# Optimization experiments

Measured on AMD Instinct MI355X. Metric: run time of the kernel, lower is better.

## Reference

```python
import jax, jax.numpy as jnp
import numpy as np

N_POI = 50000
D = 128
E = 400000
GCN_NUM = 3
HEADS = 8
B = 64
L = 100
LEAKY_SLOPE = 0.01
NORM_EPS = 1e-12


def setup_inputs() -> dict:
    key = jax.random.key(0)
    ks = jax.random.split(key, 11)
    return {
        "embeds": jax.random.normal(ks[0], (N_POI, D), jnp.float32) * 0.1,
        "gcn_W": jax.random.normal(ks[1], (GCN_NUM, D, D), jnp.float32) * (1.0 / np.sqrt(D)),
        "gcn_b": jnp.zeros((GCN_NUM, D), jnp.float32),
        "in_proj_w": jax.random.normal(ks[2], (3 * D, D), jnp.float32) * (1.0 / np.sqrt(D)),
        "in_proj_b": jnp.zeros((3 * D,), jnp.float32),
        "out_proj_w": jax.random.normal(ks[3], (D, D), jnp.float32) * (1.0 / np.sqrt(D)),
        "out_proj_b": jnp.zeros((D,), jnp.float32),
        "dist_vec": jax.random.uniform(ks[4], (E,), jnp.float32),
        "dist_edges": jax.random.randint(ks[5], (2, E), 0, N_POI),
        "x_idx": jax.random.randint(ks[6], (B * L,), 0, N_POI),
        "poi_idx": jax.random.randint(ks[7], (B,), 0, N_POI),
    }


def _self_attn(x, in_w, in_b, out_w, out_b):
    # x: [B, L, D]; standard nn.MultiheadAttention with Q=K=V=x, batch_first
    b, l, d = x.shape
    hd = d // HEADS
    qkv = x @ in_w.T + in_b                      # [B, L, 3D]
    q, k, v = jnp.split(qkv, 3, axis=-1)
    def heads(t):
        return t.reshape(b, l, HEADS, hd).transpose(0, 2, 1, 3)  # [B, H, L, hd]
    q, k, v = heads(q), heads(k), heads(v)
    scores = jnp.einsum('bhqd,bhkd->bhqk', q, k) / jnp.sqrt(jnp.asarray(hd, x.dtype))
    attn = jax.nn.softmax(scores, axis=-1)
    o = jnp.einsum('bhqk,bhkd->bhqd', attn, v).transpose(0, 2, 1, 3).reshape(b, l, d)
    return o @ out_w.T + out_b


def reference(embeds, gcn_W, gcn_b, in_proj_w, in_proj_b, out_proj_w, out_proj_b,
              dist_vec, dist_edges, x_idx, poi_idx):
    n_poi = embeds.shape[0]
    loop = jnp.arange(n_poi)
    # symmetrize edges + add self-loops (done in GeoGraph.__init__)
    rows = jnp.concatenate([dist_edges[0], dist_edges[1], loop])
    cols = jnp.concatenate([dist_edges[1], dist_edges[0], loop])
    dv = jnp.concatenate([dist_vec, dist_vec, jnp.zeros((n_poi,), dist_vec.dtype)])
    # symmetric degree normalization over destination (col) index
    deg = jax.ops.segment_sum(jnp.ones_like(dv), cols, num_segments=n_poi)
    dis = jnp.where(deg > 0, jax.lax.rsqrt(jnp.maximum(deg, 1e-12)), 0.0)
    w = jnp.exp(-dv ** 2) * dis[rows] * dis[cols]   # [E_full]

    enc = embeds
    for i in range(GCN_NUM):
        # sparse.mm: out[row] += w * enc[col]
        agg = jax.ops.segment_sum(w[:, None] * enc[cols], rows, num_segments=n_poi)
        enc = agg @ gcn_W[i].T + gcn_b[i]
        enc = jax.nn.leaky_relu(enc, LEAKY_SLOPE)
        enc = enc / jnp.maximum(jnp.linalg.norm(enc, axis=-1, keepdims=True), NORM_EPS)

    tar_embed = enc[poi_idx]                         # [B, D]
    geo_feat = enc[x_idx].reshape(B, L, D)           # equal-length sessions -> pad is a reshape
    attn_out = _self_attn(geo_feat, in_proj_w, in_proj_b, out_proj_w, out_proj_b)
    aggr_feat = attn_out.mean(axis=1)                # [B, D]
    return aggr_feat, tar_embed
```

## Files before the change

kernel.cpp:

```cpp
#include <hip/hip_runtime.h>
#include <math.h>

#define D 128
#define GCN_NUM 3
#define HEADS 8
#define HD 16
#define L_SEQ 100
#define LEAKY 0.01f
#define SC_BUCKETS 8

typedef __attribute__((ext_vector_type(8))) short short8v;
typedef __attribute__((ext_vector_type(4))) float f32x4;

__device__ __forceinline__ unsigned f2bf(float x) {
  unsigned u = __float_as_uint(x);
  return (u + 0x7FFFu + ((u >> 16) & 1u)) >> 16;
}
__device__ __forceinline__ float bflo2f(unsigned u) { return __uint_as_float(u << 16); }
__device__ __forceinline__ float bfhi2f(unsigned u) { return __uint_as_float(u & 0xFFFF0000u); }


__global__ void prep(const float* __restrict__ s0, unsigned short* __restrict__ d0, int n0,
                     const float* __restrict__ s1, unsigned short* __restrict__ d1, int n1,
                     const float* __restrict__ s2, unsigned short* __restrict__ d2, int n2,
                     int* __restrict__ deg, int N) {
  int i = blockIdx.x * blockDim.x + threadIdx.x;
  int n4tot = n0 + n1 + n2;
  if (i < n4tot) {
    const float* s; unsigned short* d; int j;
    if (i < n0)           { s = s0; d = d0; j = i; }
    else if (i < n0 + n1) { s = s1; d = d1; j = i - n0; }
    else                  { s = s2; d = d2; j = i - n0 - n1; }
    float4 v = reinterpret_cast<const float4*>(s)[j];
    uint2 o;
    o.x = f2bf(v.x) | (f2bf(v.y) << 16);
    o.y = f2bf(v.z) | (f2bf(v.w) << 16);
    reinterpret_cast<uint2*>(d)[j] = o;
  } else if (i - n4tot < N) {
    deg[i - n4tot] = 1;
  }
}


__global__ void count_deg(const int* __restrict__ e0, const int* __restrict__ e1,
                          int* __restrict__ deg, int E) {
  int stride = gridDim.x * blockDim.x;
  for (int i = blockIdx.x * blockDim.x + threadIdx.x; i < E; i += stride) {
    atomicAdd(&deg[e0[i]], 1);
    atomicAdd(&deg[e1[i]], 1);
  }
}


__global__ __launch_bounds__(1024) void block_sum(const int* __restrict__ deg,
                                                  int* __restrict__ bsum, int n) {
  __shared__ int ws[16];
  int tid = threadIdx.x, lane = tid & 63, wid = tid >> 6;
  int i = blockIdx.x * 1024 + tid;
  int v = (i < n) ? deg[i] : 0;
#pragma unroll
  for (int off = 32; off; off >>= 1) v += __shfl_xor(v, off);
  if (lane == 0) ws[wid] = v;
  __syncthreads();
  if (tid == 0) {
    int s = 0;
#pragma unroll
    for (int k = 0; k < 16; ++k) s += ws[k];
    bsum[blockIdx.x] = s;
  }
}

__global__ __launch_bounds__(1024) void scan_final(
    const int* __restrict__ deg, const int* __restrict__ bsum,
    int* __restrict__ row_ptr, int* __restrict__ cursor, int n, int nb) {
  __shared__ int ws[16];
  __shared__ int prefix_s;
  int tid = threadIdx.x, lane = tid & 63, wid = tid >> 6;
  int i = blockIdx.x * 1024 + tid;
  int v = (i < n) ? deg[i] : 0;
  int x = v;
#pragma unroll
  for (int off = 1; off < 64; off <<= 1) {
    int y = __shfl_up(x, off);
    if (lane >= off) x += y;
  }
  if (lane == 63) ws[wid] = x;
  __syncthreads();
  if (wid == 0) {
    int pv = (lane < blockIdx.x) ? bsum[lane] : 0;
#pragma unroll
    for (int off = 32; off; off >>= 1) pv += __shfl_xor(pv, off);
    if (lane == 0) prefix_s = pv;
    int s = (lane < 16) ? ws[lane] : 0;
#pragma unroll
    for (int off = 1; off < 16; off <<= 1) {
      int y = __shfl_up(s, off);
      if (lane >= off) s += y;
    }
    if (lane < 16) ws[lane] = s;
  }
  __syncthreads();
  int woff = wid ? ws[wid - 1] : 0;
  int prefix = prefix_s;
  if (i < n) {
    int pval = prefix + woff + (x - v);
    row_ptr[i] = pval;
    cursor[i] = pval;
  }
  if (blockIdx.x == nb - 1 && tid == 0) row_ptr[n] = prefix + ws[15];
}

__global__ __launch_bounds__(256) void scatter_edges_p(
    const int* __restrict__ e0, const int* __restrict__ e1,
    const float* __restrict__ dv, const int* __restrict__ deg,
    int* __restrict__ cursor, unsigned* __restrict__ ecw,
    int E, int N, int span, int bpb) {
  int bucket = blockIdx.x & (SC_BUCKETS - 1);
  int bx = blockIdx.x >> 3;
  int rlo = bucket * span;
  int rhi = min(rlo + span, N);
  int total = 2 * E + N;
  int stride = bpb * 256;
  for (int i = bx * 256 + threadIdx.x; i < total; i += stride) {
    int r, c; bool self = false;
    if (i < E)          { r = e0[i];     c = e1[i]; }
    else if (i < 2 * E) { r = e1[i - E]; c = e0[i - E]; }
    else                { r = i - 2 * E; c = r; self = true; }
    if (r < rlo || r >= rhi) continue;
    float d = self ? 0.f : dv[(i < E) ? i : i - E];
    float w = expf(-d * d) * (1.0f / sqrtf((float)deg[r])) * (1.0f / sqrtf((float)deg[c]));
    int pos = atomicAdd(&cursor[r], 1);
    ecw[pos] = (unsigned)c | (f2bf(w) << 16);
  }
}


__global__ __launch_bounds__(256) void spmm_bf(
    const int* __restrict__ row_ptr, const unsigned* __restrict__ ecw,
    const unsigned short* __restrict__ enc, unsigned short* __restrict__ agg, int n) {
  int r = blockIdx.x * 4 + (threadIdx.x >> 6);
  if (r >= n) return;
  int lane = threadIdx.x & 63;
  int g = lane >> 4, t = lane & 15;
  int s = row_ptr[r], e = row_ptr[r + 1];
  float a0 = 0.f, a1 = 0.f, a2 = 0.f, a3 = 0.f, a4 = 0.f, a5 = 0.f, a6 = 0.f, a7 = 0.f;
  int i = s + g;
  unsigned dA = 0u, dB = 0u, dC = 0u;
  if (i < e)     dA = ecw[i];
  if (i + 4 < e) dB = ecw[i + 4];
  if (i + 8 < e) dC = ecw[i + 8];
  while (i + 8 < e) {
    unsigned nA = dA, nB = dB, nC = dC;
    if (i + 12 < e) nA = ecw[i + 12];
    if (i + 16 < e) nB = ecw[i + 16];
    if (i + 20 < e) nC = ecw[i + 20];
    float wA = bfhi2f(dA), wB = bfhi2f(dB), wC = bfhi2f(dC);
    uint4 uA = *reinterpret_cast<const uint4*>(enc + (size_t)(dA & 0xFFFFu) * D + t * 8);
    uint4 uB = *reinterpret_cast<const uint4*>(enc + (size_t)(dB & 0xFFFFu) * D + t * 8);
    uint4 uC = *reinterpret_cast<const uint4*>(enc + (size_t)(dC & 0xFFFFu) * D + t * 8);
    a0 = fmaf(wA, bflo2f(uA.x), a0); a1 = fmaf(wA, bfhi2f(uA.x), a1);
    a2 = fmaf(wA, bflo2f(uA.y), a2); a3 = fmaf(wA, bfhi2f(uA.y), a3);
    a4 = fmaf(wA, bflo2f(uA.z), a4); a5 = fmaf(wA, bfhi2f(uA.z), a5);
    a6 = fmaf(wA, bflo2f(uA.w), a6); a7 = fmaf(wA, bfhi2f(uA.w), a7);
    a0 = fmaf(wB, bflo2f(uB.x), a0); a1 = fmaf(wB, bfhi2f(uB.x), a1);
    a2 = fmaf(wB, bflo2f(uB.y), a2); a3 = fmaf(wB, bfhi2f(uB.y), a3);
    a4 = fmaf(wB, bflo2f(uB.z), a4); a5 = fmaf(wB, bfhi2f(uB.z), a5);
    a6 = fmaf(wB, bflo2f(uB.w), a6); a7 = fmaf(wB, bfhi2f(uB.w), a7);
    a0 = fmaf(wC, bflo2f(uC.x), a0); a1 = fmaf(wC, bfhi2f(uC.x), a1);
    a2 = fmaf(wC, bflo2f(uC.y), a2); a3 = fmaf(wC, bfhi2f(uC.y), a3);
    a4 = fmaf(wC, bflo2f(uC.z), a4); a5 = fmaf(wC, bfhi2f(uC.z), a5);
    a6 = fmaf(wC, bflo2f(uC.w), a6); a7 = fmaf(wC, bfhi2f(uC.w), a7);
    dA = nA; dB = nB; dC = nC;
    i += 12;
  }
  if (i < e) {
    float wA = bfhi2f(dA);
    uint4 uA = *reinterpret_cast<const uint4*>(enc + (size_t)(dA & 0xFFFFu) * D + t * 8);
    a0 = fmaf(wA, bflo2f(uA.x), a0); a1 = fmaf(wA, bfhi2f(uA.x), a1);
    a2 = fmaf(wA, bflo2f(uA.y), a2); a3 = fmaf(wA, bfhi2f(uA.y), a3);
    a4 = fmaf(wA, bflo2f(uA.z), a4); a5 = fmaf(wA, bfhi2f(uA.z), a5);
    a6 = fmaf(wA, bflo2f(uA.w), a6); a7 = fmaf(wA, bfhi2f(uA.w), a7);
  }
  if (i + 4 < e) {
    float wB = bfhi2f(dB);
    uint4 uB = *reinterpret_cast<const uint4*>(enc + (size_t)(dB & 0xFFFFu) * D + t * 8);
    a0 = fmaf(wB, bflo2f(uB.x), a0); a1 = fmaf(wB, bfhi2f(uB.x), a1);
    a2 = fmaf(wB, bflo2f(uB.y), a2); a3 = fmaf(wB, bfhi2f(uB.y), a3);
    a4 = fmaf(wB, bflo2f(uB.z), a4); a5 = fmaf(wB, bfhi2f(uB.z), a5);
    a6 = fmaf(wB, bflo2f(uB.w), a6); a7 = fmaf(wB, bfhi2f(uB.w), a7);
  }
  a0 += __shfl_xor(a0, 16); a0 += __shfl_xor(a0, 32);
  a1 += __shfl_xor(a1, 16); a1 += __shfl_xor(a1, 32);
  a2 += __shfl_xor(a2, 16); a2 += __shfl_xor(a2, 32);
  a3 += __shfl_xor(a3, 16); a3 += __shfl_xor(a3, 32);
  a4 += __shfl_xor(a4, 16); a4 += __shfl_xor(a4, 32);
  a5 += __shfl_xor(a5, 16); a5 += __shfl_xor(a5, 32);
  a6 += __shfl_xor(a6, 16); a6 += __shfl_xor(a6, 32);
  a7 += __shfl_xor(a7, 16); a7 += __shfl_xor(a7, 32);
  if (g == 0) {
    uint4 o;
    o.x = f2bf(a0) | (f2bf(a1) << 16);
    o.y = f2bf(a2) | (f2bf(a3) << 16);
    o.z = f2bf(a4) | (f2bf(a5) << 16);
    o.w = f2bf(a6) | (f2bf(a7) << 16);
    *reinterpret_cast<uint4*>(agg + (size_t)r * D + t * 8) = o;
  }
}

__global__ __launch_bounds__(256) void dense_mfma(
    const unsigned short* __restrict__ A, const unsigned short* __restrict__ Wb,
    const float* __restrict__ bias, unsigned short* __restrict__ enc, int n) {
  __shared__ unsigned short Wl[128 * 136];
  int tid = threadIdx.x;
  {
    int cg = (tid & 15) * 8;
    int r0 = tid >> 4;
#pragma unroll
    for (int i = 0; i < 8; ++i) {
      int row = r0 + i * 16;
      *reinterpret_cast<short8v*>(&Wl[row * 136 + cg]) =
          *reinterpret_cast<const short8v*>(Wb + row * D + cg);
    }
  }
  __syncthreads();
  int w = tid >> 6, lane = tid & 63;
  int lr = lane & 15, lg = lane >> 4;
#pragma unroll
  for (int rt = 0; rt < 2; ++rt) {
    int rbase = blockIdx.x * 128 + rt * 64 + w * 16;
    f32x4 acc[8];
#pragma unroll
    for (int j = 0; j < 8; ++j) acc[j] = f32x4{0.f, 0.f, 0.f, 0.f};
    const unsigned short* arow = A + (size_t)(rbase + lr) * D + lg * 8;
#pragma unroll
    for (int ks = 0; ks < 4; ++ks) {
      short8v a = *reinterpret_cast<const short8v*>(arow + ks * 32);
#pragma unroll
      for (int jt = 0; jt < 8; ++jt) {
        short8v b = *reinterpret_cast<const short8v*>(&Wl[(jt * 16 + lr) * 136 + ks * 32 + lg * 8]);
        acc[jt] = __builtin_amdgcn_mfma_f32_16x16x32_bf16(a, b, acc[jt], 0, 0, 0);
      }
    }
    float vals[8][4];
    float ss[4] = {0.f, 0.f, 0.f, 0.f};
#pragma unroll
    for (int jt = 0; jt < 8; ++jt) {
      float bj = bias[jt * 16 + lr];
#pragma unroll
      for (int i = 0; i < 4; ++i) {
        float t = acc[jt][i] + bj;
        t = (t > 0.f) ? t : LEAKY * t;
        vals[jt][i] = t;
        ss[i] += t * t;
      }
    }
#pragma unroll
    for (int i = 0; i < 4; ++i) {
      float s = ss[i];
      s += __shfl_xor(s, 1); s += __shfl_xor(s, 2);
      s += __shfl_xor(s, 4); s += __shfl_xor(s, 8);
      ss[i] = 1.0f / fmaxf(sqrtf(s), 1e-12f);
    }
#pragma unroll
    for (int i = 0; i < 4; ++i) {
      int row = rbase + lg * 4 + i;
      if (row < n) {
#pragma unroll
        for (int jt = 0; jt < 8; ++jt)
          enc[(size_t)row * D + jt * 16 + lr] = (unsigned short)f2bf(vals[jt][i] * ss[i]);
      }
    }
  }
}


__global__ void gather_tar(const unsigned short* __restrict__ src,
                           const int* __restrict__ poi_idx, float* __restrict__ tar, int B) {
  int j = blockIdx.x;
  if (j < B) {
    int t = threadIdx.x;
    unsigned u = reinterpret_cast<const unsigned*>(src + (size_t)poi_idx[j] * D)[t];
    reinterpret_cast<float2*>(tar + (size_t)j * D)[t] = make_float2(bflo2f(u), bfhi2f(u));
  }
}

__global__ __launch_bounds__(256) void qkv_mfma(
    const unsigned short* __restrict__ enc, const int* __restrict__ x_idx,
    const unsigned short* __restrict__ Wb, const float* __restrict__ bias,
    float* __restrict__ qkv, int M) {
  __shared__ unsigned short Wl[128 * 136];
  int tid = threadIdx.x;
  const unsigned short* Wslab = Wb + (size_t)blockIdx.y * 128 * D;
  {
    int cg = (tid & 15) * 8;
    int r0 = tid >> 4;
#pragma unroll
    for (int i = 0; i < 8; ++i) {
      int row = r0 + i * 16;
      *reinterpret_cast<short8v*>(&Wl[row * 136 + cg]) =
          *reinterpret_cast<const short8v*>(Wslab + row * D + cg);
    }
  }
  __syncthreads();
  int w = tid >> 6, lane = tid & 63;
  int lr = lane & 15, lg = lane >> 4;
  int colbase = blockIdx.y * 128;
#pragma unroll
  for (int rt = 0; rt < 2; ++rt) {
    int rbase = blockIdx.x * 128 + rt * 64 + w * 16;
    f32x4 acc[8];
#pragma unroll
    for (int j = 0; j < 8; ++j) acc[j] = f32x4{0.f, 0.f, 0.f, 0.f};
    const unsigned short* arow = enc + (size_t)x_idx[rbase + lr] * D + lg * 8;
#pragma unroll
    for (int ks = 0; ks < 4; ++ks) {
      short8v a = *reinterpret_cast<const short8v*>(arow + ks * 32);
#pragma unroll
      for (int jt = 0; jt < 8; ++jt) {
        short8v b = *reinterpret_cast<const short8v*>(&Wl[(jt * 16 + lr) * 136 + ks * 32 + lg * 8]);
        acc[jt] = __builtin_amdgcn_mfma_f32_16x16x32_bf16(a, b, acc[jt], 0, 0, 0);
      }
    }
#pragma unroll
    for (int jt = 0; jt < 8; ++jt) {
      int j = colbase + jt * 16 + lr;
      float bj = bias[j];
#pragma unroll
      for (int i = 0; i < 4; ++i) {
        int row = rbase + lg * 4 + i;
        if (row < M) qkv[(size_t)row * 384 + j] = acc[jt][i] + bj;
      }
    }
  }
}

__global__ __launch_bounds__(128) void attn_kernel(
    const float* __restrict__ qkv, float* __restrict__ o) {
  __shared__ float k_s[L_SEQ][HD];
  __shared__ float v_s[L_SEQ][HD];
  __shared__ float sc[L_SEQ][L_SEQ + 1];
  int b = blockIdx.x / HEADS;
  int h = blockIdx.x % HEADS;
  int tid = threadIdx.x;
  const size_t rowbase = (size_t)b * L_SEQ;
  for (int idx = tid; idx < L_SEQ * HD; idx += 128) {
    int l = idx >> 4, d2 = idx & 15;
    const float* base = qkv + (rowbase + l) * 384 + h * HD + d2;
    k_s[l][d2] = base[128];
    v_s[l][d2] = base[256];
  }
  __syncthreads();
  if (tid < L_SEQ) {
    float q[HD];
    const float* qp = qkv + (rowbase + tid) * 384 + h * HD;
#pragma unroll
    for (int d2 = 0; d2 < HD; ++d2) q[d2] = qp[d2];
    float m = -1e30f;
    for (int j = 0; j < L_SEQ; ++j) {
      float s = 0.f;
#pragma unroll
      for (int d2 = 0; d2 < HD; ++d2) s += q[d2] * k_s[j][d2];
      s *= 0.25f;
      sc[tid][j] = s;
      m = fmaxf(m, s);
    }
    float sum = 0.f;
    for (int j = 0; j < L_SEQ; ++j) {
      float e = expf(sc[tid][j] - m);
      sc[tid][j] = e;
      sum += e;
    }
    float inv = 1.f / sum;
    float oacc[HD];
#pragma unroll
    for (int d2 = 0; d2 < HD; ++d2) oacc[d2] = 0.f;
    for (int j = 0; j < L_SEQ; ++j) {
      float p = sc[tid][j];
#pragma unroll
      for (int d2 = 0; d2 < HD; ++d2) oacc[d2] += p * v_s[j][d2];
    }
    float* op = o + (rowbase + tid) * D + h * HD;
#pragma unroll
    for (int d2 = 0; d2 < HD; ++d2) op[d2] = oacc[d2] * inv;
  }
}

__global__ __launch_bounds__(128) void out_mean_kernel(
    const float* __restrict__ o, const float* __restrict__ Wo,
    const float* __restrict__ bo, float* __restrict__ out, int L) {
  __shared__ float m_s[D];
  int b = blockIdx.x, tid = threadIdx.x;
  float s = 0.f;
  for (int l = 0; l < L; ++l) s += o[((size_t)b * L + l) * D + tid];
  m_s[tid] = s / (float)L;
  __syncthreads();
  const float4* w4 = reinterpret_cast<const float4*>(Wo + (size_t)tid * D);
  float acc = 0.f;
  for (int k4 = 0; k4 < D / 4; ++k4) {
    float4 w = w4[k4];
    int k = k4 * 4;
    acc += m_s[k] * w.x + m_s[k + 1] * w.y + m_s[k + 2] * w.z + m_s[k + 3] * w.w;
  }
  out[(size_t)b * D + tid] = acc + bo[tid];
}


extern "C" void kernel_launch(void* const* d_in, const int* in_sizes, int n_in,
                              void* d_out, int out_size, void* d_ws, size_t ws_size,
                              hipStream_t stream) {
  const float* embeds   = (const float*)d_in[0];
  const float* gcn_W    = (const float*)d_in[1];
  const float* gcn_b    = (const float*)d_in[2];
  const float* in_w     = (const float*)d_in[3];
  const float* in_b     = (const float*)d_in[4];
  const float* out_w    = (const float*)d_in[5];
  const float* out_b    = (const float*)d_in[6];
  const float* dist_vec = (const float*)d_in[7];
  const int*   edges    = (const int*)d_in[8];
  const int*   x_idx    = (const int*)d_in[9];
  const int*   poi_idx  = (const int*)d_in[10];
  float* out = (float*)d_out;

  int N  = in_sizes[0] / D;
  int E  = in_sizes[7];
  int BL = in_sizes[9];
  int B  = in_sizes[10];
  int L  = BL / B;
  const int* e0 = edges;
  const int* e1 = edges + E;
  size_t total_edges = (size_t)2 * E + N;
  int Npad = ((N + 127) / 128) * 128;
  int NB   = (N + 1023) / 1024;

  char* p = (char*)d_ws;
  auto alloc = [&](size_t bytes) { char* q = p; p += (bytes + 255) & ~(size_t)255; return q; };
  int*      deg     = (int*)alloc((size_t)N * 4);
  int*      row_ptr = (int*)alloc((size_t)(N + 1) * 4);
  int*      cursor  = (int*)alloc((size_t)N * 4);
  int*      bsum    = (int*)alloc((size_t)NB * 4);
  unsigned* ecw     = (unsigned*)alloc(total_edges * 4);
  unsigned short* emb_bf = (unsigned short*)alloc((size_t)Npad * D * 2);
  unsigned short* W_bf   = (unsigned short*)alloc((size_t)GCN_NUM * D * D * 2);
  unsigned short* inw_bf = (unsigned short*)alloc((size_t)3 * D * D * 2);
  unsigned short* agg_bf = (unsigned short*)alloc((size_t)Npad * D * 2);
  unsigned short* enc_bf = (unsigned short*)alloc((size_t)Npad * D * 2);
  float* qkv  = (float*)alloc((size_t)BL * 384 * 4);
  float* obuf = (float*)alloc((size_t)BL * D * 4);

  int n4e = N * D / 4, n4w = GCN_NUM * D * D / 4, n4i = 3 * D * D / 4;
  int prep_tot = n4e + n4w + n4i + N;
  prep<<<(prep_tot + 255) / 256, 256, 0, stream>>>(
      embeds, emb_bf, n4e, gcn_W, W_bf, n4w, in_w, inw_bf, n4i, deg, N);

  count_deg<<<1024, 256, 0, stream>>>(e0, e1, deg, E);
  block_sum<<<NB, 1024, 0, stream>>>(deg, bsum, N);
  scan_final<<<NB, 1024, 0, stream>>>(deg, bsum, row_ptr, cursor, N, NB);
  int span = (N + SC_BUCKETS - 1) / SC_BUCKETS;
  int bpb = 512;
  scatter_edges_p<<<SC_BUCKETS * bpb, 256, 0, stream>>>(
      e0, e1, dist_vec, deg, cursor, ecw, E, N, span, bpb);

  const unsigned short* cur_in = emb_bf;
  for (int i = 0; i < GCN_NUM; ++i) {
    spmm_bf<<<(N + 3) / 4, 256, 0, stream>>>(row_ptr, ecw, cur_in, agg_bf, N);
    dense_mfma<<<Npad / 128, 256, 0, stream>>>(
        agg_bf, W_bf + (size_t)i * D * D, gcn_b + (size_t)i * D, enc_bf, N);
    cur_in = enc_bf;
  }

  gather_tar<<<B, 64, 0, stream>>>(enc_bf, poi_idx, out + (size_t)B * D, B);
  dim3 qgrid(BL / 128, 3);
  qkv_mfma<<<qgrid, 256, 0, stream>>>(enc_bf, x_idx, inw_bf, in_b, qkv, BL);
  attn_kernel<<<B * HEADS, 128, 0, stream>>>(qkv, obuf);
  out_mean_kernel<<<B, 128, 0, stream>>>(obuf, out_w, out_b, out, L);
}
```

Measured before the change: 358.1 us.

## Fuse sparse aggregation and dense GCN layer into one kernel

Merges the per-row SpMM gather with the MFMA dense transform, LeakyReLU and L2 normalisation into a single kernel per layer. Each block aggregates 64 rows at a time into shared memory and then runs the matmul on that tile. Ping-pong encoding buffers replace the intermediate aggregate buffer. This removes the global write and re-read of the aggregate tensor and one launch per layer. In exchange, the grid shrinks from thousands of small blocks to a few hundred large ones, and each wave walks 16 rows in sequence, which reduces the parallelism available to hide gather latency.

```diff
diff --git a/kernel.cpp b/kernel.cpp
--- a/kernel.cpp
+++ b/kernel.cpp
@@ -50,7 +50,6 @@
     atomicAdd(&deg[e1[i]], 1);
   }
 }
-
 
 __global__ __launch_bounds__(1024) void block_sum(const int* __restrict__ deg,
                                                   int* __restrict__ bsum, int n) {
@@ -134,83 +133,15 @@
   }
 }
 
-
-__global__ __launch_bounds__(256) void spmm_bf(
+__global__ __launch_bounds__(256) void layer_fused(
     const int* __restrict__ row_ptr, const unsigned* __restrict__ ecw,
-    const unsigned short* __restrict__ enc, unsigned short* __restrict__ agg, int n) {
-  int r = blockIdx.x * 4 + (threadIdx.x >> 6);
-  if (r >= n) return;
-  int lane = threadIdx.x & 63;
-  int g = lane >> 4, t = lane & 15;
-  int s = row_ptr[r], e = row_ptr[r + 1];
-  float a0 = 0.f, a1 = 0.f, a2 = 0.f, a3 = 0.f, a4 = 0.f, a5 = 0.f, a6 = 0.f, a7 = 0.f;
-  int i = s + g;
-  unsigned dA = 0u, dB = 0u, dC = 0u;
-  if (i < e)     dA = ecw[i];
-  if (i + 4 < e) dB = ecw[i + 4];
-  if (i + 8 < e) dC = ecw[i + 8];
-  while (i + 8 < e) {
-    unsigned nA = dA, nB = dB, nC = dC;
-    if (i + 12 < e) nA = ecw[i + 12];
-    if (i + 16 < e) nB = ecw[i + 16];
-    if (i + 20 < e) nC = ecw[i + 20];
-    float wA = bfhi2f(dA), wB = bfhi2f(dB), wC = bfhi2f(dC);
-    uint4 uA = *reinterpret_cast<const uint4*>(enc + (size_t)(dA & 0xFFFFu) * D + t * 8);
-    uint4 uB = *reinterpret_cast<const uint4*>(enc + (size_t)(dB & 0xFFFFu) * D + t * 8);
-    uint4 uC = *reinterpret_cast<const uint4*>(enc + (size_t)(dC & 0xFFFFu) * D + t * 8);
-    a0 = fmaf(wA, bflo2f(uA.x), a0); a1 = fmaf(wA, bfhi2f(uA.x), a1);
-    a2 = fmaf(wA, bflo2f(uA.y), a2); a3 = fmaf(wA, bfhi2f(uA.y), a3);
-    a4 = fmaf(wA, bflo2f(uA.z), a4); a5 = fmaf(wA, bfhi2f(uA.z), a5);
-    a6 = fmaf(wA, bflo2f(uA.w), a6); a7 = fmaf(wA, bfhi2f(uA.w), a7);
-    a0 = fmaf(wB, bflo2f(uB.x), a0); a1 = fmaf(wB, bfhi2f(uB.x), a1);
-    a2 = fmaf(wB, bflo2f(uB.y), a2); a3 = fmaf(wB, bfhi2f(uB.y), a3);
-    a4 = fmaf(wB, bflo2f(uB.z), a4); a5 = fmaf(wB, bfhi2f(uB.z), a5);
-    a6 = fmaf(wB, bflo2f(uB.w), a6); a7 = fmaf(wB, bfhi2f(uB.w), a7);
-    a0 = fmaf(wC, bflo2f(uC.x), a0); a1 = fmaf(wC, bfhi2f(uC.x), a1);
-    a2 = fmaf(wC, bflo2f(uC.y), a2); a3 = fmaf(wC, bfhi2f(uC.y), a3);
-    a4 = fmaf(wC, bflo2f(uC.z), a4); a5 = fmaf(wC, bfhi2f(uC.z), a5);
-    a6 = fmaf(wC, bflo2f(uC.w), a6); a7 = fmaf(wC, bfhi2f(uC.w), a7);
-    dA = nA; dB = nB; dC = nC;
-    i += 12;
-  }
-  if (i < e) {
-    float wA = bfhi2f(dA);
-    uint4 uA = *reinterpret_cast<const uint4*>(enc + (size_t)(dA & 0xFFFFu) * D + t * 8);
-    a0 = fmaf(wA, bflo2f(uA.x), a0); a1 = fmaf(wA, bfhi2f(uA.x), a1);
-    a2 = fmaf(wA, bflo2f(uA.y), a2); a3 = fmaf(wA, bfhi2f(uA.y), a3);
-    a4 = fmaf(wA, bflo2f(uA.z), a4); a5 = fmaf(wA, bfhi2f(uA.z), a5);
-    a6 = fmaf(wA, bflo2f(uA.w), a6); a7 = fmaf(wA, bfhi2f(uA.w), a7);
-  }
-  if (i + 4 < e) {
-    float wB = bfhi2f(dB);
-    uint4 uB = *reinterpret_cast<const uint4*>(enc + (size_t)(dB & 0xFFFFu) * D + t * 8);
-    a0 = fmaf(wB, bflo2f(uB.x), a0); a1 = fmaf(wB, bfhi2f(uB.x), a1);
-    a2 = fmaf(wB, bflo2f(uB.y), a2); a3 = fmaf(wB, bfhi2f(uB.y), a3);
-    a4 = fmaf(wB, bflo2f(uB.z), a4); a5 = fmaf(wB, bfhi2f(uB.z), a5);
-    a6 = fmaf(wB, bflo2f(uB.w), a6); a7 = fmaf(wB, bfhi2f(uB.w), a7);
-  }
-  a0 += __shfl_xor(a0, 16); a0 += __shfl_xor(a0, 32);
-  a1 += __shfl_xor(a1, 16); a1 += __shfl_xor(a1, 32);
-  a2 += __shfl_xor(a2, 16); a2 += __shfl_xor(a2, 32);
-  a3 += __shfl_xor(a3, 16); a3 += __shfl_xor(a3, 32);
-  a4 += __shfl_xor(a4, 16); a4 += __shfl_xor(a4, 32);
-  a5 += __shfl_xor(a5, 16); a5 += __shfl_xor(a5, 32);
-  a6 += __shfl_xor(a6, 16); a6 += __shfl_xor(a6, 32);
-  a7 += __shfl_xor(a7, 16); a7 += __shfl_xor(a7, 32);
-  if (g == 0) {
-    uint4 o;
-    o.x = f2bf(a0) | (f2bf(a1) << 16);
-    o.y = f2bf(a2) | (f2bf(a3) << 16);
-    o.z = f2bf(a4) | (f2bf(a5) << 16);
-    o.w = f2bf(a6) | (f2bf(a7) << 16);
-    *reinterpret_cast<uint4*>(agg + (size_t)r * D + t * 8) = o;
-  }
-}
-
-__global__ __launch_bounds__(256) void dense_mfma(
-    const unsigned short* __restrict__ A, const unsigned short* __restrict__ Wb,
-    const float* __restrict__ bias, unsigned short* __restrict__ enc, int n) {
+    const unsigned short* __restrict__ enc_in,
+    const unsigned short* __restrict__ Wb,
+    const float* __restrict__ bias,
+    unsigned short* __restrict__ enc_out,
+    int n) {
   __shared__ unsigned short Wl[128 * 136];
+  __shared__ unsigned short As[64 * 136];
   int tid = threadIdx.x;
   {
     int cg = (tid & 15) * 8;
@@ -222,19 +153,89 @@
           *reinterpret_cast<const short8v*>(Wb + row * D + cg);
     }
   }
-  __syncthreads();
   int w = tid >> 6, lane = tid & 63;
+  int g = lane >> 4, t = lane & 15;
   int lr = lane & 15, lg = lane >> 4;
-#pragma unroll
-  for (int rt = 0; rt < 2; ++rt) {
-    int rbase = blockIdx.x * 128 + rt * 64 + w * 16;
+
+#pragma unroll
+  for (int half = 0; half < 2; ++half) {
+    __syncthreads();
+    for (int k = 0; k < 16; ++k) {
+      int lrow = w * 16 + k;
+      int r = blockIdx.x * 128 + half * 64 + lrow;
+      int s = 0, e = 0;
+      if (r < n) { s = row_ptr[r]; e = row_ptr[r + 1]; }
+      float a0 = 0.f, a1 = 0.f, a2 = 0.f, a3 = 0.f, a4 = 0.f, a5 = 0.f, a6 = 0.f, a7 = 0.f;
+      int i = s + g;
+      unsigned dA = 0u, dB = 0u, dC = 0u;
+      if (i < e)     dA = ecw[i];
+      if (i + 4 < e) dB = ecw[i + 4];
+      if (i + 8 < e) dC = ecw[i + 8];
+      while (i + 8 < e) {
+        unsigned nA = dA, nB = dB, nC = dC;
+        if (i + 12 < e) nA = ecw[i + 12];
+        if (i + 16 < e) nB = ecw[i + 16];
+        if (i + 20 < e) nC = ecw[i + 20];
+        float wA = bfhi2f(dA), wB = bfhi2f(dB), wC = bfhi2f(dC);
+        uint4 uA = *reinterpret_cast<const uint4*>(enc_in + (size_t)(dA & 0xFFFFu) * D + t * 8);
+        uint4 uB = *reinterpret_cast<const uint4*>(enc_in + (size_t)(dB & 0xFFFFu) * D + t * 8);
+        uint4 uC = *reinterpret_cast<const uint4*>(enc_in + (size_t)(dC & 0xFFFFu) * D + t * 8);
+        a0 = fmaf(wA, bflo2f(uA.x), a0); a1 = fmaf(wA, bfhi2f(uA.x), a1);
+        a2 = fmaf(wA, bflo2f(uA.y), a2); a3 = fmaf(wA, bfhi2f(uA.y), a3);
+        a4 = fmaf(wA, bflo2f(uA.z), a4); a5 = fmaf(wA, bfhi2f(uA.z), a5);
+        a6 = fmaf(wA, bflo2f(uA.w), a6); a7 = fmaf(wA, bfhi2f(uA.w), a7);
+        a0 = fmaf(wB, bflo2f(uB.x), a0); a1 = fmaf(wB, bfhi2f(uB.x), a1);
+        a2 = fmaf(wB, bflo2f(uB.y), a2); a3 = fmaf(wB, bfhi2f(uB.y), a3);
+        a4 = fmaf(wB, bflo2f(uB.z), a4); a5 = fmaf(wB, bfhi2f(uB.z), a5);
+        a6 = fmaf(wB, bflo2f(uB.w), a6); a7 = fmaf(wB, bfhi2f(uB.w), a7);
+        a0 = fmaf(wC, bflo2f(uC.x), a0); a1 = fmaf(wC, bfhi2f(uC.x), a1);
+        a2 = fmaf(wC, bflo2f(uC.y), a2); a3 = fmaf(wC, bfhi2f(uC.y), a3);
+        a4 = fmaf(wC, bflo2f(uC.z), a4); a5 = fmaf(wC, bfhi2f(uC.z), a5);
+        a6 = fmaf(wC, bflo2f(uC.w), a6); a7 = fmaf(wC, bfhi2f(uC.w), a7);
+        dA = nA; dB = nB; dC = nC;
+        i += 12;
+      }
+      if (i < e) {
+        float wA = bfhi2f(dA);
+        uint4 uA = *reinterpret_cast<const uint4*>(enc_in + (size_t)(dA & 0xFFFFu) * D + t * 8);
+        a0 = fmaf(wA, bflo2f(uA.x), a0); a1 = fmaf(wA, bfhi2f(uA.x), a1);
+        a2 = fmaf(wA, bflo2f(uA.y), a2); a3 = fmaf(wA, bfhi2f(uA.y), a3);
+        a4 = fmaf(wA, bflo2f(uA.z), a4); a5 = fmaf(wA, bfhi2f(uA.z), a5);
+        a6 = fmaf(wA, bflo2f(uA.w), a6); a7 = fmaf(wA, bfhi2f(uA.w), a7);
+      }
+      if (i + 4 < e) {
+        float wB = bfhi2f(dB);
+        uint4 uB = *reinterpret_cast<const uint4*>(enc_in + (size_t)(dB & 0xFFFFu) * D + t * 8);
+        a0 = fmaf(wB, bflo2f(uB.x), a0); a1 = fmaf(wB, bfhi2f(uB.x), a1);
+        a2 = fmaf(wB, bflo2f(uB.y), a2); a3 = fmaf(wB, bfhi2f(uB.y), a3);
+        a4 = fmaf(wB, bflo2f(uB.z), a4); a5 = fmaf(wB, bfhi2f(uB.z), a5);
+        a6 = fmaf(wB, bflo2f(uB.w), a6); a7 = fmaf(wB, bfhi2f(uB.w), a7);
+      }
+      a0 += __shfl_xor(a0, 16); a0 += __shfl_xor(a0, 32);
+      a1 += __shfl_xor(a1, 16); a1 += __shfl_xor(a1, 32);
+      a2 += __shfl_xor(a2, 16); a2 += __shfl_xor(a2, 32);
+      a3 += __shfl_xor(a3, 16); a3 += __shfl_xor(a3, 32);
+      a4 += __shfl_xor(a4, 16); a4 += __shfl_xor(a4, 32);
+      a5 += __shfl_xor(a5, 16); a5 += __shfl_xor(a5, 32);
+      a6 += __shfl_xor(a6, 16); a6 += __shfl_xor(a6, 32);
+      a7 += __shfl_xor(a7, 16); a7 += __shfl_xor(a7, 32);
+      if (g == 0) {
+        uint4 o;
+        o.x = f2bf(a0) | (f2bf(a1) << 16);
+        o.y = f2bf(a2) | (f2bf(a3) << 16);
+        o.z = f2bf(a4) | (f2bf(a5) << 16);
+        o.w = f2bf(a6) | (f2bf(a7) << 16);
+        *reinterpret_cast<uint4*>(&As[lrow * 136 + t * 8]) = o;
+      }
+    }
+    __syncthreads();
+    int rbase = blockIdx.x * 128 + half * 64 + w * 16;
     f32x4 acc[8];
 #pragma unroll
     for (int j = 0; j < 8; ++j) acc[j] = f32x4{0.f, 0.f, 0.f, 0.f};
-    const unsigned short* arow = A + (size_t)(rbase + lr) * D + lg * 8;
 #pragma unroll
     for (int ks = 0; ks < 4; ++ks) {
-      short8v a = *reinterpret_cast<const short8v*>(arow + ks * 32);
+      short8v a = *reinterpret_cast<const short8v*>(&As[(w * 16 + lr) * 136 + ks * 32 + lg * 8]);
 #pragma unroll
       for (int jt = 0; jt < 8; ++jt) {
         short8v b = *reinterpret_cast<const short8v*>(&Wl[(jt * 16 + lr) * 136 + ks * 32 + lg * 8]);
@@ -248,10 +249,10 @@
       float bj = bias[jt * 16 + lr];
 #pragma unroll
       for (int i = 0; i < 4; ++i) {
-        float t = acc[jt][i] + bj;
-        t = (t > 0.f) ? t : LEAKY * t;
-        vals[jt][i] = t;
-        ss[i] += t * t;
+        float tv = acc[jt][i] + bj;
+        tv = (tv > 0.f) ? tv : LEAKY * tv;
+        vals[jt][i] = tv;
+        ss[i] += tv * tv;
       }
     }
 #pragma unroll
@@ -267,7 +268,7 @@
       if (row < n) {
 #pragma unroll
         for (int jt = 0; jt < 8; ++jt)
-          enc[(size_t)row * D + jt * 16 + lr] = (unsigned short)f2bf(vals[jt][i] * ss[i]);
+          enc_out[(size_t)row * D + jt * 16 + lr] = (unsigned short)f2bf(vals[jt][i] * ss[i]);
       }
     }
   }
@@ -442,8 +443,8 @@
   unsigned short* emb_bf = (unsigned short*)alloc((size_t)Npad * D * 2);
   unsigned short* W_bf   = (unsigned short*)alloc((size_t)GCN_NUM * D * D * 2);
   unsigned short* inw_bf = (unsigned short*)alloc((size_t)3 * D * D * 2);
-  unsigned short* agg_bf = (unsigned short*)alloc((size_t)Npad * D * 2);
-  unsigned short* enc_bf = (unsigned short*)alloc((size_t)Npad * D * 2);
+  unsigned short* enc_a  = (unsigned short*)alloc((size_t)Npad * D * 2);
+  unsigned short* enc_b  = (unsigned short*)alloc((size_t)Npad * D * 2);
   float* qkv  = (float*)alloc((size_t)BL * 384 * 4);
   float* obuf = (float*)alloc((size_t)BL * D * 4);
 
@@ -460,17 +461,17 @@
   scatter_edges_p<<<SC_BUCKETS * bpb, 256, 0, stream>>>(
       e0, e1, dist_vec, deg, cursor, ecw, E, N, span, bpb);
 
-  const unsigned short* cur_in = emb_bf;
-  for (int i = 0; i < GCN_NUM; ++i) {
-    spmm_bf<<<(N + 3) / 4, 256, 0, stream>>>(row_ptr, ecw, cur_in, agg_bf, N);
-    dense_mfma<<<Npad / 128, 256, 0, stream>>>(
-        agg_bf, W_bf + (size_t)i * D * D, gcn_b + (size_t)i * D, enc_bf, N);
-    cur_in = enc_bf;
-  }
-
-  gather_tar<<<B, 64, 0, stream>>>(enc_bf, poi_idx, out + (size_t)B * D, B);
+  int lgrid = Npad / 128;
+  layer_fused<<<lgrid, 256, 0, stream>>>(row_ptr, ecw, emb_bf,
+      W_bf + 0 * (size_t)D * D, gcn_b + 0 * (size_t)D, enc_a, N);
+  layer_fused<<<lgrid, 256, 0, stream>>>(row_ptr, ecw, enc_a,
+      W_bf + 1 * (size_t)D * D, gcn_b + 1 * (size_t)D, enc_b, N);
+  layer_fused<<<lgrid, 256, 0, stream>>>(row_ptr, ecw, enc_b,
+      W_bf + 2 * (size_t)D * D, gcn_b + 2 * (size_t)D, enc_a, N);
+
+  gather_tar<<<B, 64, 0, stream>>>(enc_a, poi_idx, out + (size_t)B * D, B);
   dim3 qgrid(BL / 128, 3);
-  qkv_mfma<<<qgrid, 256, 0, stream>>>(enc_bf, x_idx, inw_bf, in_b, qkv, BL);
+  qkv_mfma<<<qgrid, 256, 0, stream>>>(enc_a, x_idx, inw_bf, in_b, qkv, BL);
   attn_kernel<<<B * HEADS, 128, 0, stream>>>(qkv, obuf);
   out_mean_kernel<<<B, 128, 0, stream>>>(obuf, out_w, out_b, out, L);
 }
```

Result: slower. 471.0 us (+31.5%).
